# Kernel optimization log

Hardware: AMD Instinct MI355X
Metric: run time of the kernel (lower is better)

The kernel has to match this reference:

```python
import jax, jax.numpy as jnp
import numpy as np


def _quat_raw_mul(a, b):
    aw, ax, ay, az = a[..., 0], a[..., 1], a[..., 2], a[..., 3]
    bw, bx, by, bz = b[..., 0], b[..., 1], b[..., 2], b[..., 3]
    ow = aw * bw - ax * bx - ay * by - az * bz
    ox = aw * bx + ax * bw + ay * bz - az * by
    oy = aw * by - ax * bz + ay * bw + az * bx
    oz = aw * bz + ax * by - ay * bx + az * bw
    return jnp.stack([ow, ox, oy, oz], axis=-1)


def _standardize(q):
    # pytorch3d.quaternion_multiply standardizes sign so w >= 0
    return jnp.where(q[..., :1] < 0, -q, q)


def _quat_apply(q, v):
    # rotate points v by unit quaternions q: q * (0, v) * conj(q), take imaginary part
    pv = jnp.concatenate([jnp.zeros_like(v[..., :1]), v], axis=-1)
    conj = q * jnp.asarray([1.0, -1.0, -1.0, -1.0], dtype=q.dtype)
    return _quat_raw_mul(_quat_raw_mul(q, pv), conj)[..., 1:]


def _axis_angle_to_quat(aa):
    # pytorch3d.axis_angle_to_quaternion with small-angle Taylor branch
    angle = jnp.linalg.norm(aa, axis=-1, keepdims=True)
    half = 0.5 * angle
    eps = 1e-6
    small = jnp.abs(angle) < eps
    safe_angle = jnp.where(small, jnp.ones_like(angle), angle)
    k = jnp.where(small, 0.5 - angle * angle / 48.0, jnp.sin(half) / safe_angle)
    return jnp.concatenate([jnp.cos(half), aa * k], axis=-1)


def _matrix_to_quat(M):
    # pytorch3d.matrix_to_quaternion (candidate-selection form), vectorized
    m00, m11, m22 = M[..., 0, 0], M[..., 1, 1], M[..., 2, 2]
    q_abs = jnp.sqrt(jax.nn.relu(jnp.stack([
        1.0 + m00 + m11 + m22,
        1.0 + m00 - m11 - m22,
        1.0 - m00 + m11 - m22,
        1.0 - m00 - m11 + m22], axis=-1)))
    c0 = jnp.stack([q_abs[..., 0] ** 2, M[..., 2, 1] - M[..., 1, 2], M[..., 0, 2] - M[..., 2, 0], M[..., 1, 0] - M[..., 0, 1]], axis=-1)
    c1 = jnp.stack([M[..., 2, 1] - M[..., 1, 2], q_abs[..., 1] ** 2, M[..., 1, 0] + M[..., 0, 1], M[..., 0, 2] + M[..., 2, 0]], axis=-1)
    c2 = jnp.stack([M[..., 0, 2] - M[..., 2, 0], M[..., 1, 0] + M[..., 0, 1], q_abs[..., 2] ** 2, M[..., 2, 1] + M[..., 1, 2]], axis=-1)
    c3 = jnp.stack([M[..., 1, 0] - M[..., 0, 1], M[..., 2, 0] + M[..., 0, 2], M[..., 2, 1] + M[..., 1, 2], q_abs[..., 3] ** 2], axis=-1)
    cands = jnp.stack([c0, c1, c2, c3], axis=-2)  # (..., 4 candidates, 4)
    flr = 0.1
    cands = cands / (2.0 * jnp.maximum(q_abs[..., None], flr))
    idx = jnp.argmax(q_abs, axis=-1)
    return jnp.take_along_axis(cands, idx[..., None, None], axis=-2)[..., 0, :]


def _or6d_to_quat(d6):
    a1, a2 = d6[..., :3], d6[..., 3:]
    b1 = a1 / jnp.linalg.norm(a1, axis=-1, keepdims=True)
    a2p = a2 - jnp.sum(b1 * a2, axis=-1, keepdims=True) * b1
    b2 = a2p / jnp.linalg.norm(a2p, axis=-1, keepdims=True)
    b3 = jnp.cross(b1, b2)
    M = jnp.stack([b1, b2, b3], axis=-2)  # (..., 3, 3)
    return _matrix_to_quat(M)


def setup_inputs() -> dict:
    key = jax.random.key(0)
    k1, k2, k3, k4 = jax.random.split(key, 4)
    N, T, J = 256, 1024, 24
    return {
        'root_rvel': jax.random.normal(k1, (N, T, 1, 1), dtype=jnp.float32),
        'local_pos': jax.random.normal(k2, (N, T + 1, J, 3), dtype=jnp.float32),
        'local_rot': jax.random.normal(k3, (N, T + 1, J, 6), dtype=jnp.float32),
        'root_vel': jax.random.normal(k4, (N, T, 1, 2), dtype=jnp.float32),
    }


def reference(root_rvel, local_pos, local_rot, root_vel):
    # cumulative root yaw angle with zero initial frame: (N, T+1, 1, 1)
    r = jnp.cumsum(root_rvel, axis=1)
    r = jnp.concatenate([jnp.zeros_like(r[:, :1]), r], axis=1)
    # axis-angle about Y axis -> quaternion (N, T+1, 1, 4)
    aa = r * jnp.asarray([0.0, 1.0, 0.0], dtype=r.dtype)
    rotation = _axis_angle_to_quat(aa)
    # local 6D rotations -> quaternions (N, T+1, J, 4)
    local_q = _or6d_to_quat(local_rot)
    global_rot = _standardize(_quat_raw_mul(rotation, local_q))
    relative_pos = _quat_apply(rotation, local_pos)
    # lift XZ hip velocity to 3D, rotate into world frame, integrate
    zeros_y = jnp.zeros_like(root_vel[..., :1])
    v3 = jnp.concatenate([root_vel[..., :1], zeros_y, root_vel[..., 1:]], axis=-1)  # (N,T,1,3)
    v3w = _quat_apply(rotation[:, :-1], v3)
    pos_xz = jnp.concatenate([jnp.zeros_like(v3w[:, :1]), jnp.cumsum(v3w, axis=1)], axis=1)  # (N,T+1,1,3)
    global_pos = relative_pos + pos_xz
    return global_pos, global_rot
```

## Files before the change

kernel.cpp:

```cpp
#include <hip/hip_runtime.h>

#define N_SEQ 256
#define T_LEN 1024
#define TP1   (T_LEN + 1)
#define J_NUM 24
#define ITEMS (TP1 * J_NUM)
#define GP_TOTAL (N_SEQ * TP1 * J_NUM * 3)

__device__ __forceinline__ float block_scan_incl(float v, float* wsum, int tid) {
    const int lane = tid & 63;
    const int wid  = tid >> 6;
    #pragma unroll
    for (int off = 1; off < 64; off <<= 1) {
        float u = __shfl_up(v, off, 64);
        if (lane >= off) v += u;
    }
    if (lane == 63) wsum[wid] = v;
    __syncthreads();
    if (tid == 0) {
        float acc = 0.0f;
        #pragma unroll
        for (int i = 0; i < 16; ++i) { float t = wsum[i]; wsum[i] = acc; acc += t; }
    }
    __syncthreads();
    return v + wsum[wid];
}

extern "C" __global__ void __launch_bounds__(1024)
unprocess_kernel(const float* __restrict__ root_rvel,
                 const float* __restrict__ local_pos,
                 const float* __restrict__ local_rot,
                 const float* __restrict__ root_vel,
                 float* __restrict__ out_pos,
                 float* __restrict__ out_rot)
{
    const int n   = blockIdx.x;
    const int tid = threadIdx.x;

    __shared__ float  r_s[TP1];
    __shared__ float2 quat_s[TP1];
    __shared__ float2 pos_s[TP1];
    __shared__ float  ws_a[16], ws_b[16], ws_c[16];

    {
        float v = root_rvel[n * T_LEN + tid];
        float incl = block_scan_incl(v, ws_a, tid);
        if (tid == 0) r_s[0] = 0.0f;
        r_s[tid + 1] = incl;
    }
    __syncthreads();

    for (int idx = tid; idx < TP1; idx += 1024) {
        float r     = r_s[idx];
        float angle = fabsf(r);
        float half  = 0.5f * angle;
        float k = (angle < 1e-6f) ? (0.5f - angle * angle * (1.0f / 48.0f))
                                  : (__builtin_sinf(half) / angle);
        quat_s[idx] = make_float2(__builtin_cosf(half), r * k);
    }
    __syncthreads();

    {
        float2 vel = ((const float2*)root_vel)[n * T_LEN + tid];
        float2 q   = quat_s[tid];
        float  w = q.x, y = q.y;
        float t1x = w * vel.x + y * vel.y;
        float t1z = w * vel.y - y * vel.x;
        float ax  = t1x * w + t1z * y;
        float az  = t1z * w - t1x * y;
        float ix = block_scan_incl(ax, ws_b, tid);
        float iz = block_scan_incl(az, ws_c, tid);
        if (tid == 0) pos_s[0] = make_float2(0.0f, 0.0f);
        pos_s[tid + 1] = make_float2(ix, iz);
    }
    __syncthreads();

    const long long item_base = (long long)n * ITEMS;
    for (int idx = tid; idx < ITEMS; idx += 1024) {
        const int t = idx / J_NUM;
        const long long item = item_base + idx;

        const float* rp = local_rot + item * 6;
        float2 d01 = *(const float2*)(rp + 0);
        float2 d23 = *(const float2*)(rp + 2);
        float2 d45 = *(const float2*)(rp + 4);
        float a1x = d01.x, a1y = d01.y, a1z = d23.x;
        float a2x = d23.y, a2y = d45.x, a2z = d45.y;

        float inv1 = 1.0f / sqrtf(a1x * a1x + a1y * a1y + a1z * a1z);
        float b1x = a1x * inv1, b1y = a1y * inv1, b1z = a1z * inv1;
        float dp  = b1x * a2x + b1y * a2y + b1z * a2z;
        float px  = a2x - dp * b1x, py = a2y - dp * b1y, pz = a2z - dp * b1z;
        float inv2 = 1.0f / sqrtf(px * px + py * py + pz * pz);
        float b2x = px * inv2, b2y = py * inv2, b2z = pz * inv2;
        float b3x = b1y * b2z - b1z * b2y;
        float b3y = b1z * b2x - b1x * b2z;
        float b3z = b1x * b2y - b1y * b2x;
        float m00 = b1x, m01 = b1y, m02 = b1z;
        float m10 = b2x, m11 = b2y, m12 = b2z;
        float m20 = b3x, m21 = b3y, m22 = b3z;

        float qa0 = sqrtf(fmaxf(1.0f + m00 + m11 + m22, 0.0f));
        float qa1 = sqrtf(fmaxf(1.0f + m00 - m11 - m22, 0.0f));
        float qa2 = sqrtf(fmaxf(1.0f - m00 + m11 - m22, 0.0f));
        float qa3 = sqrtf(fmaxf(1.0f - m00 - m11 + m22, 0.0f));

        int best = 0; float bv = qa0;
        if (qa1 > bv) { best = 1; bv = qa1; }
        if (qa2 > bv) { best = 2; bv = qa2; }
        if (qa3 > bv) { best = 3; bv = qa3; }

        float lw, lx, ly, lz;
        if (best == 0)      { lw = qa0 * qa0;  lx = m21 - m12;  ly = m02 - m20;  lz = m10 - m01; }
        else if (best == 1) { lw = m21 - m12;  lx = qa1 * qa1;  ly = m10 + m01;  lz = m02 + m20; }
        else if (best == 2) { lw = m02 - m20;  lx = m10 + m01;  ly = qa2 * qa2;  lz = m21 + m12; }
        else                { lw = m10 - m01;  lx = m20 + m02;  ly = m21 + m12;  lz = qa3 * qa3; }
        float invd = 1.0f / (2.0f * fmaxf(bv, 0.1f));
        lw *= invd; lx *= invd; ly *= invd; lz *= invd;

        float2 qt = quat_s[t];
        float w = qt.x, yq = qt.y;
        float ow = w * lw - yq * ly;
        float ox = w * lx + yq * lz;
        float oy = w * ly + yq * lw;
        float oz = w * lz - yq * lx;
        if (ow < 0.0f) { ow = -ow; ox = -ox; oy = -oy; oz = -oz; }
        *(float4*)(out_rot + item * 4) = make_float4(ow, ox, oy, oz);

        const float* pp = local_pos + item * 3;
        float vx = pp[0], vy = pp[1], vz = pp[2];
        float t1x = w * vx + yq * vz;
        float t1z = w * vz - yq * vx;
        float rx = t1x * w + t1z * yq;
        float ry = (w * w + yq * yq) * vy;
        float rz = t1z * w - t1x * yq;
        float2 ps = pos_s[t];
        out_pos[item * 3 + 0] = rx + ps.x;
        out_pos[item * 3 + 1] = ry;
        out_pos[item * 3 + 2] = rz + ps.y;
    }
}

extern "C" void kernel_launch(void* const* d_in, const int* in_sizes, int n_in,
                              void* d_out, int out_size, void* d_ws, size_t ws_size,
                              hipStream_t stream) {
    (void)in_sizes; (void)n_in; (void)d_ws; (void)ws_size; (void)out_size;
    const float* root_rvel = (const float*)d_in[0];
    const float* local_pos = (const float*)d_in[1];
    const float* local_rot = (const float*)d_in[2];
    const float* root_vel  = (const float*)d_in[3];
    float* out = (float*)d_out;
    unprocess_kernel<<<N_SEQ, 1024, 0, stream>>>(
        root_rvel, local_pos, local_rot, root_vel, out, out + GP_TOTAL);
}
```

Before: 348.4 us.

## Split scan and elementwise work into two kernels with vectorized float4 IO

Moves the per-sequence prefix scans into a small kernel that writes root quaternions and integrated positions to workspace. A second, fully parallel kernel then processes four joints per thread using float4 loads and stores. This removes the one-block-per-sequence limit on occupancy and the strided scalar memory traffic. The cost is an extra launch and a round trip through workspace for the per-frame data.

Measured after the change: 349.6 us. No clear change (+0.4%).

```diff
diff --git a/kernel.cpp b/kernel.cpp
--- a/kernel.cpp
+++ b/kernel.cpp
@@ -5,6 +5,8 @@
 #define TP1   (T_LEN + 1)
 #define J_NUM 24
 #define ITEMS (TP1 * J_NUM)
+#define TOTAL_ITEMS (N_SEQ * ITEMS)
+#define TOTAL_GROUPS (TOTAL_ITEMS / 4)
 #define GP_TOTAL (N_SEQ * TP1 * J_NUM * 3)
 
 __device__ __forceinline__ float block_scan_incl(float v, float* wsum, int tid) {
@@ -27,19 +29,16 @@
 }
 
 extern "C" __global__ void __launch_bounds__(1024)
-unprocess_kernel(const float* __restrict__ root_rvel,
-                 const float* __restrict__ local_pos,
-                 const float* __restrict__ local_rot,
-                 const float* __restrict__ root_vel,
-                 float* __restrict__ out_pos,
-                 float* __restrict__ out_rot)
+scan_kernel(const float* __restrict__ root_rvel,
+            const float* __restrict__ root_vel,
+            float2* __restrict__ ws_quat,
+            float2* __restrict__ ws_pos)
 {
     const int n   = blockIdx.x;
     const int tid = threadIdx.x;
 
     __shared__ float  r_s[TP1];
     __shared__ float2 quat_s[TP1];
-    __shared__ float2 pos_s[TP1];
     __shared__ float  ws_a[16], ws_b[16], ws_c[16];
 
     {
@@ -56,7 +55,9 @@
         float half  = 0.5f * angle;
         float k = (angle < 1e-6f) ? (0.5f - angle * angle * (1.0f / 48.0f))
                                   : (__builtin_sinf(half) / angle);
-        quat_s[idx] = make_float2(__builtin_cosf(half), r * k);
+        float2 q = make_float2(__builtin_cosf(half), r * k);
+        quat_s[idx] = q;
+        ws_quat[n * TP1 + idx] = q;
     }
     __syncthreads();
 
@@ -70,22 +71,52 @@
         float az  = t1z * w - t1x * y;
         float ix = block_scan_incl(ax, ws_b, tid);
         float iz = block_scan_incl(az, ws_c, tid);
-        if (tid == 0) pos_s[0] = make_float2(0.0f, 0.0f);
-        pos_s[tid + 1] = make_float2(ix, iz);
+        if (tid == 0) ws_pos[n * TP1] = make_float2(0.0f, 0.0f);
+        ws_pos[n * TP1 + tid + 1] = make_float2(ix, iz);
     }
-    __syncthreads();
+}
 
-    const long long item_base = (long long)n * ITEMS;
-    for (int idx = tid; idx < ITEMS; idx += 1024) {
-        const int t = idx / J_NUM;
-        const long long item = item_base + idx;
+extern "C" __global__ void __launch_bounds__(256)
+elem_kernel(const float4* __restrict__ rot4,
+            const float4* __restrict__ pos4,
+            const float2* __restrict__ ws_quat,
+            const float2* __restrict__ ws_pos,
+            float4* __restrict__ out_rot4,
+            float4* __restrict__ out_pos4)
+{
+    const unsigned g = blockIdx.x * 256u + threadIdx.x;
+    if (g >= TOTAL_GROUPS) return;
+    const unsigned base = g * 4u;
+    const unsigned seq  = base / ITEMS;
+    const unsigned t    = (base - seq * ITEMS) / J_NUM;
 
-        const float* rp = local_rot + item * 6;
-        float2 d01 = *(const float2*)(rp + 0);
-        float2 d23 = *(const float2*)(rp + 2);
-        float2 d45 = *(const float2*)(rp + 4);
-        float a1x = d01.x, a1y = d01.y, a1z = d23.x;
-        float a2x = d23.y, a2y = d45.x, a2z = d45.y;
+    const float2 qt = ws_quat[seq * TP1 + t];
+    const float2 ps = ws_pos [seq * TP1 + t];
+    const float w = qt.x, yq = qt.y;
+    const float wwyy = w * w + yq * yq;
+
+    float rf[24], pf[12], opf[12];
+    {
+        const float4* rp = rot4 + (size_t)g * 6;
+        #pragma unroll
+        for (int i = 0; i < 6; ++i) {
+            float4 a = rp[i];
+            rf[4*i+0] = a.x; rf[4*i+1] = a.y; rf[4*i+2] = a.z; rf[4*i+3] = a.w;
+        }
+        const float4* pp = pos4 + (size_t)g * 3;
+        #pragma unroll
+        for (int i = 0; i < 3; ++i) {
+            float4 a = pp[i];
+            pf[4*i+0] = a.x; pf[4*i+1] = a.y; pf[4*i+2] = a.z; pf[4*i+3] = a.w;
+        }
+    }
+
+    float4* orp = out_rot4 + (size_t)g * 4;
+
+    #pragma unroll
+    for (int k = 0; k < 4; ++k) {
+        float a1x = rf[6*k+0], a1y = rf[6*k+1], a1z = rf[6*k+2];
+        float a2x = rf[6*k+3], a2y = rf[6*k+4], a2z = rf[6*k+5];
 
         float inv1 = 1.0f / sqrtf(a1x * a1x + a1y * a1y + a1z * a1z);
         float b1x = a1x * inv1, b1y = a1y * inv1, b1z = a1z * inv1;
@@ -96,6 +127,7 @@
         float b3x = b1y * b2z - b1z * b2y;
         float b3y = b1z * b2x - b1x * b2z;
         float b3z = b1x * b2y - b1y * b2x;
+
         float m00 = b1x, m01 = b1y, m02 = b1z;
         float m10 = b2x, m11 = b2y, m12 = b2z;
         float m20 = b3x, m21 = b3y, m22 = b3z;
@@ -118,38 +150,45 @@
         float invd = 1.0f / (2.0f * fmaxf(bv, 0.1f));
         lw *= invd; lx *= invd; ly *= invd; lz *= invd;
 
-        float2 qt = quat_s[t];
-        float w = qt.x, yq = qt.y;
         float ow = w * lw - yq * ly;
         float ox = w * lx + yq * lz;
         float oy = w * ly + yq * lw;
         float oz = w * lz - yq * lx;
         if (ow < 0.0f) { ow = -ow; ox = -ox; oy = -oy; oz = -oz; }
-        *(float4*)(out_rot + item * 4) = make_float4(ow, ox, oy, oz);
+        orp[k] = make_float4(ow, ox, oy, oz);
 
-        const float* pp = local_pos + item * 3;
-        float vx = pp[0], vy = pp[1], vz = pp[2];
+        float vx = pf[3*k+0], vy = pf[3*k+1], vz = pf[3*k+2];
         float t1x = w * vx + yq * vz;
         float t1z = w * vz - yq * vx;
-        float rx = t1x * w + t1z * yq;
-        float ry = (w * w + yq * yq) * vy;
-        float rz = t1z * w - t1x * yq;
-        float2 ps = pos_s[t];
-        out_pos[item * 3 + 0] = rx + ps.x;
-        out_pos[item * 3 + 1] = ry;
-        out_pos[item * 3 + 2] = rz + ps.y;
+        opf[3*k+0] = t1x * w + t1z * yq + ps.x;
+        opf[3*k+1] = wwyy * vy;
+        opf[3*k+2] = t1z * w - t1x * yq + ps.y;
     }
+
+    float4* opp = out_pos4 + (size_t)g * 3;
+    #pragma unroll
+    for (int i = 0; i < 3; ++i)
+        opp[i] = make_float4(opf[4*i+0], opf[4*i+1], opf[4*i+2], opf[4*i+3]);
 }
 
 extern "C" void kernel_launch(void* const* d_in, const int* in_sizes, int n_in,
                               void* d_out, int out_size, void* d_ws, size_t ws_size,
                               hipStream_t stream) {
-    (void)in_sizes; (void)n_in; (void)d_ws; (void)ws_size; (void)out_size;
+    (void)in_sizes; (void)n_in; (void)ws_size; (void)out_size;
     const float* root_rvel = (const float*)d_in[0];
     const float* local_pos = (const float*)d_in[1];
     const float* local_rot = (const float*)d_in[2];
     const float* root_vel  = (const float*)d_in[3];
     float* out = (float*)d_out;
-    unprocess_kernel<<<N_SEQ, 1024, 0, stream>>>(
-        root_rvel, local_pos, local_rot, root_vel, out, out + GP_TOTAL);
+
+    float2* ws_quat = (float2*)d_ws;
+    float2* ws_pos  = ws_quat + (size_t)N_SEQ * TP1;
+
+    scan_kernel<<<N_SEQ, 1024, 0, stream>>>(root_rvel, root_vel, ws_quat, ws_pos);
+
+    elem_kernel<<<TOTAL_GROUPS / 256, 256, 0, stream>>>(
+        (const float4*)local_rot, (const float4*)local_pos,
+        ws_quat, ws_pos,
+        (float4*)(out + GP_TOTAL),
+        (float4*)out);
 }
```
